# Optimization experiments

Hardware: AMD Instinct MI355X
Metric: run time of the kernel (lower is better)

## Reference

```python
import jax, jax.numpy as jnp
import numpy as np

T, B, K, H = 2048, 4, 512, 8  # seq_len, batch, num_features, num_heads


def setup_inputs() -> dict:
    key = jax.random.key(0)
    ks = jax.random.split(key, 9)
    s_in = 1.0 / np.sqrt(K).astype(np.float32)       # torch Linear init bound (fan_in = K)
    s_out = 1.0 / np.sqrt(H * K).astype(np.float32)  # fan_in = H*K for output linear
    u = lambda k, shape, s: jax.random.uniform(k, shape, jnp.float32, -s, s)
    return {
        "x": jax.random.normal(ks[0], (T, B, K), jnp.float32),
        "Wq": u(ks[1], (K, H * K), s_in), "bq": u(ks[2], (H * K,), s_in),
        "Wk": u(ks[3], (K, H * K), s_in), "bk": u(ks[4], (H * K,), s_in),
        "Wv": u(ks[5], (K, H * K), s_in), "bv": u(ks[6], (H * K,), s_in),
        "Wo": u(ks[7], (H * K, H), s_out), "bo": u(ks[8], (H,), s_out),
    }


def reference(x, Wq, bq, Wk, bk, Wv, bv, Wo, bo):
    t, b, k = x.shape
    h = Wq.shape[1] // k
    scale = k ** -0.25  # q and k each scaled by num_features**(1/4) -> net 1/sqrt(k)
    # QKV projections: (t, b, h*k) -> view as (t, b*h, k) like the torch .view
    q = ((jnp.einsum('tbk,kf->tbf', x, Wq) + bq) * scale).reshape(t, b * h, k)
    ky = ((jnp.einsum('tbk,kf->tbf', x, Wk) + bk) * scale).reshape(t, b * h, k)
    v = (jnp.einsum('tbk,kf->tbf', x, Wv) + bv).reshape(t, b * h, k)
    # per-(batch*head) slice attention, vectorized over the b*h axis n
    scores = jnp.einsum('tnk,snk->nts', q, ky)          # (b*h, t, t)
    attn = jax.nn.softmax(scores, axis=-1)
    ctx = jnp.einsum('nts,snk->tnk', attn, v).reshape(t, b, h * k)
    return jnp.einsum('tbf,fo->tbo', ctx, Wo) + bo      # (t, b, h)
```

## Files before the change

### kernel.cpp

```cpp
#include <hip/hip_runtime.h>
#include <hip/hip_bf16.h>
#include <stdint.h>


typedef __bf16 bf16_t;
typedef __bf16 bf16x8 __attribute__((ext_vector_type(8)));
using short8 = __attribute__((ext_vector_type(8))) short;
typedef float  f32x4  __attribute__((ext_vector_type(4)));
typedef uint32_t u32;

#define T_N 2048
#define K_N 512
#define F_N 4096
#define SCALE_QK 0.21022410381342863f

#define AS3 __attribute__((address_space(3)))
#define AS1 __attribute__((address_space(1)))

__device__ __forceinline__ void gll16(const void* gsrc, void* ldst) {
  __builtin_amdgcn_global_load_lds((const AS1 u32*)gsrc, (AS3 u32*)ldst, 16, 0, 0);
}

__global__ void prep_x(const float* __restrict__ x, bf16_t* __restrict__ xb) {
  int i = (blockIdx.x * 256 + threadIdx.x) * 8;
  float4 a = *(const float4*)(x + i);
  float4 b = *(const float4*)(x + i + 4);
  bf16x8 o;
  o[0] = (bf16_t)a.x; o[1] = (bf16_t)a.y; o[2] = (bf16_t)a.z; o[3] = (bf16_t)a.w;
  o[4] = (bf16_t)b.x; o[5] = (bf16_t)b.y; o[6] = (bf16_t)b.z; o[7] = (bf16_t)b.w;
  *(bf16x8*)(xb + i) = o;
}

__global__ void prep_w(const float* __restrict__ Wq, const float* __restrict__ Wk,
                       const float* __restrict__ Wv, bf16_t* __restrict__ Wt) {
  const float* W = blockIdx.z == 0 ? Wq : (blockIdx.z == 1 ? Wk : Wv);
  bf16_t* out = Wt + (size_t)blockIdx.z * F_N * K_N;
  __shared__ alignas(16) bf16_t tile[64][72];
  int k0 = blockIdx.x * 64, f0 = blockIdx.y * 64;
  int tid = threadIdx.x;
  int r = tid >> 3, cc = (tid & 7) * 8;
#pragma unroll
  for (int h = 0; h < 2; h++) {
    int rr = r + h * 32;
    const float* src = W + (size_t)(k0 + rr) * F_N + f0 + cc;
    float4 a = *(const float4*)src;
    float4 b = *(const float4*)(src + 4);
    bf16_t* d = &tile[rr][cc];
    d[0] = (bf16_t)a.x; d[1] = (bf16_t)a.y; d[2] = (bf16_t)a.z; d[3] = (bf16_t)a.w;
    d[4] = (bf16_t)b.x; d[5] = (bf16_t)b.y; d[6] = (bf16_t)b.z; d[7] = (bf16_t)b.w;
  }
  __syncthreads();
#pragma unroll
  for (int h = 0; h < 2; h++) {
    int rr = r + h * 32;
    bf16x8 o;
#pragma unroll
    for (int j = 0; j < 8; j++) o[j] = tile[cc + j][rr];
    *(bf16x8*)(out + (size_t)(f0 + rr) * K_N + k0 + cc) = o;
  }
}

__global__ void zero_l(float* l) { l[blockIdx.x * 256 + threadIdx.x] = 0.0f; }

template <int CHH>
__global__ void transpose_v_t(const bf16_t* __restrict__ Vc, bf16_t* __restrict__ Vtc) {
  constexpr int CW = CHH * 512;
  int zc = blockIdx.z, b = zc & 3, hh = zc >> 2;
  int t0 = blockIdx.x * 64, d0 = blockIdx.y * 64;
  __shared__ alignas(16) bf16_t tile[64][72];
  int tid = threadIdx.x;
  int r = tid >> 3, cc = (tid & 7) * 8;
#pragma unroll
  for (int h = 0; h < 2; h++) {
    int rr = r + h * 32;
    *(bf16x8*)&tile[rr][cc] = *(const bf16x8*)(
        Vc + (size_t)(t0 + rr) * 4 * CW + (size_t)b * CW + hh * 512 + d0 + cc);
  }
  __syncthreads();
  bf16_t* out = Vtc + (size_t)zc * K_N * T_N;
#pragma unroll
  for (int h = 0; h < 2; h++) {
    int rr = r + h * 32;
    bf16x8 o;
#pragma unroll
    for (int j = 0; j < 8; j++) o[j] = tile[cc + j][rr];
    *(bf16x8*)(out + (size_t)(d0 + rr) * T_N + t0 + cc) = o;
  }
}

struct GemmAcc { f32x4 a[4][4]; };

__device__ __forceinline__ void gemm_bt_core(
    const char* __restrict__ Ab, size_t sA, const char* __restrict__ Bb, size_t sB,
    int mbase, int nbase, int NK, char* smem, GemmAcc& G) {
  const int tid = threadIdx.x;
  const int lane = tid & 63;
  const int wid = tid >> 6;
#pragma unroll
  for (int i = 0; i < 4; i++)
#pragma unroll
    for (int j = 0; j < 4; j++) G.a[i][j] = f32x4{0.f, 0.f, 0.f, 0.f};

  const int rsub = lane >> 3;
  const int qb = (lane & 7) * 16;

  auto stage = [&](int buf, int kt) {
    char* base = smem + buf * 32768;
#pragma unroll
    for (int it = 0; it < 4; it++) {
      int r = wid * 32 + it * 8 + rsub;
      const char* src = Ab + (size_t)(mbase + r) * sA + kt * 128 + (qb ^ ((r & 7) << 4));
      gll16(src, base + wid * 4096 + it * 1024);
    }
#pragma unroll
    for (int it = 0; it < 4; it++) {
      int r = wid * 32 + it * 8 + rsub;
      const char* src = Bb + (size_t)(nbase + r) * sB + kt * 128 + (qb ^ ((r & 7) << 4));
      gll16(src, base + 16384 + wid * 4096 + it * 1024);
    }
  };

  const int wm = wid >> 1, wn = wid & 1;
  const int rl = lane & 15;
  const int kg = (lane >> 4) * 16;

  auto compute = [&](int buf) {
    const char* base = smem + buf * 32768;
#pragma unroll
    for (int kf = 0; kf < 2; kf++) {
      int kb = kf * 64 + kg;
      short8 af[4], bfv[4];
#pragma unroll
      for (int mf = 0; mf < 4; mf++) {
        int m = wm * 64 + mf * 16 + rl;
        af[mf] = *(const short8*)(base + m * 128 + (kb ^ ((m & 7) << 4)));
      }
#pragma unroll
      for (int nf = 0; nf < 4; nf++) {
        int n = wn * 64 + nf * 16 + rl;
        bfv[nf] = *(const short8*)(base + 16384 + n * 128 + (kb ^ ((n & 7) << 4)));
      }
#pragma unroll
      for (int mf = 0; mf < 4; mf++)
#pragma unroll
        for (int nf = 0; nf < 4; nf++)
          G.a[mf][nf] = __builtin_amdgcn_mfma_f32_16x16x32_bf16(af[mf], bfv[nf],
                                                                G.a[mf][nf], 0, 0, 0);
    }
  };

  stage(0, 0);
  for (int kt = 0; kt < NK; kt++) {
    __syncthreads();
    if (kt + 1 < NK) stage((kt + 1) & 1, kt + 1);
    compute(kt & 1);
  }
}

#define EPILOGUE_COORDS                                   \
  const int lane = threadIdx.x & 63;                      \
  const int wid = threadIdx.x >> 6;                       \
  const int wm = wid >> 1, wn = wid & 1;                  \
  const int cl = lane & 15;                               \
  const int rg = (lane >> 4) * 4;

template <int CHH>
__global__ __launch_bounds__(256, 2) void gemm_proj_t(
    const bf16_t* __restrict__ xb, const bf16_t* __restrict__ Wt,
    bf16_t* __restrict__ Qc, bf16_t* __restrict__ Kc, bf16_t* __restrict__ Vc,
    const float* __restrict__ bq, const float* __restrict__ bk,
    const float* __restrict__ bv, int h0) {
  constexpr int CW = CHH * 512;
  __shared__ alignas(16) char smem[65536];
  int z = blockIdx.z;
  const char* Ab = (const char*)xb;
  const char* Bb = (const char*)(Wt + ((size_t)z * F_N + h0 * 512) * K_N);
  int mbase = blockIdx.x * 128, nbase = blockIdx.y * 128;
  GemmAcc G;
  gemm_bt_core(Ab, 1024, Bb, 1024, mbase, nbase, 8, smem, G);

  bf16_t* C = z == 0 ? Qc : (z == 1 ? Kc : Vc);
  const float* bias = z == 0 ? bq : (z == 1 ? bk : bv);
  float scale = z < 2 ? SCALE_QK : 1.0f;
  EPILOGUE_COORDS
#pragma unroll
  for (int nf = 0; nf < 4; nf++) {
    int col = nbase + wn * 64 + nf * 16 + cl;
    float bvv = bias[h0 * 512 + col];
#pragma unroll
    for (int mf = 0; mf < 4; mf++)
#pragma unroll
      for (int ri = 0; ri < 4; ri++) {
        int row = mbase + wm * 64 + mf * 16 + rg + ri;
        C[(size_t)row * CW + col] = (bf16_t)((G.a[mf][nf][ri] + bvv) * scale);
      }
  }
}

template <int CHH>
__global__ __launch_bounds__(256, 2) void gemm_s_t(
    const bf16_t* __restrict__ Qc, const bf16_t* __restrict__ Kc,
    bf16_t* __restrict__ E, float* __restrict__ L, int h0, int zb) {
  constexpr int CW = CHH * 512;
  __shared__ alignas(16) char smem[65536];
  int ze = blockIdx.z;
  int zc = zb + ze, b = zc & 3, hh = zc >> 2;
  const char* Ab = (const char*)(Qc + (size_t)(b * CHH + hh) * 512);
  const char* Bb = (const char*)(Kc + (size_t)(b * CHH + hh) * 512);
  int mbase = blockIdx.x * 128, nbase = blockIdx.y * 128;
  GemmAcc G;
  gemm_bt_core(Ab, 8 * CW, Bb, 8 * CW, mbase, nbase, 8, smem, G);

  bf16_t* C = E + (size_t)ze * T_N * T_N;
  float* Ln = L + ((h0 + hh) * 4 + b) * T_N;
  EPILOGUE_COORDS
#pragma unroll
  for (int mf = 0; mf < 4; mf++)
#pragma unroll
    for (int ri = 0; ri < 4; ri++) {
      int row = mbase + wm * 64 + mf * 16 + rg + ri;
      float rs = 0.0f;
#pragma unroll
      for (int nf = 0; nf < 4; nf++) {
        int col = nbase + wn * 64 + nf * 16 + cl;
        float e = __expf(G.a[mf][nf][ri]);
        rs += e;
        C[(size_t)row * T_N + col] = (bf16_t)e;
      }
#pragma unroll
      for (int off = 1; off < 16; off <<= 1) rs += __shfl_xor(rs, off, 16);
      if ((lane & 15) == 0) atomicAdd(Ln + row, rs);
    }
}

template <int CHH>
__global__ __launch_bounds__(256, 2) void gemm_pv_t(
    const bf16_t* __restrict__ E, const bf16_t* __restrict__ Vtc,
    const float* __restrict__ L, bf16_t* __restrict__ ctxc, int h0, int zb) {
  constexpr int CW = CHH * 512;
  __shared__ alignas(16) char smem[65536];
  int ze = blockIdx.z;
  int zc = zb + ze, b = zc & 3, hh = zc >> 2;
  const char* Ab = (const char*)(E + (size_t)ze * T_N * T_N);
  const char* Bb = (const char*)(Vtc + (size_t)zc * K_N * T_N);
  int mbase = blockIdx.x * 128, nbase = blockIdx.y * 128;
  GemmAcc G;
  gemm_bt_core(Ab, 4096, Bb, 4096, mbase, nbase, 32, smem, G);

  const float* Ln = L + ((h0 + hh) * 4 + b) * T_N;
  bf16_t* C = ctxc + (size_t)(b * CHH + hh) * 512;
  EPILOGUE_COORDS
#pragma unroll
  for (int mf = 0; mf < 4; mf++)
#pragma unroll
    for (int ri = 0; ri < 4; ri++) {
      int row = mbase + wm * 64 + mf * 16 + rg + ri;
      float inv = 1.0f / Ln[row];
#pragma unroll
      for (int nf = 0; nf < 4; nf++) {
        int col = nbase + wn * 64 + nf * 16 + cl;
        C[(size_t)row * 4 * CW + col] = (bf16_t)(G.a[mf][nf][ri] * inv);
      }
    }
}

template <int CHH>
__global__ __launch_bounds__(256) void out_gemm_t(
    const bf16_t* __restrict__ ctxc, const float* __restrict__ Wo,
    const float* __restrict__ bo, float* __restrict__ out, int h0, int first) {
  constexpr int CW = CHH * 512;
  int tid = threadIdx.x, lane = tid & 63, wid = tid >> 6;
  int r = blockIdx.x * 4 + wid;
  const bf16_t* crow = ctxc + (size_t)r * CW + lane * (8 * CHH);
  const float* wbase = Wo + ((size_t)h0 * 512 + lane * (8 * CHH)) * 8;
  float p[8];
#pragma unroll
  for (int o = 0; o < 8; o++) p[o] = 0.0f;
#pragma unroll
  for (int j = 0; j < 8 * CHH; j += 8) {
    bf16x8 cv = *(const bf16x8*)(crow + j);
#pragma unroll
    for (int u = 0; u < 8; u++) {
      float c = (float)cv[u];
      const float* wrow = wbase + (j + u) * 8;
      f32x4 w0 = *(const f32x4*)wrow;
      f32x4 w1 = *(const f32x4*)(wrow + 4);
      p[0] += c * w0[0]; p[1] += c * w0[1]; p[2] += c * w0[2]; p[3] += c * w0[3];
      p[4] += c * w1[0]; p[5] += c * w1[1]; p[6] += c * w1[2]; p[7] += c * w1[3];
    }
  }
#pragma unroll
  for (int off = 1; off < 64; off <<= 1)
#pragma unroll
    for (int o = 0; o < 8; o++) p[o] += __shfl_xor(p[o], off, 64);
  if (lane == 0) {
#pragma unroll
    for (int o = 0; o < 8; o++) {
      float base = first ? bo[o] : out[r * 8 + o];
      out[r * 8 + o] = base + p[o];
    }
  }
}

template <int CHH>
static void run_chunks(const bf16_t* xb, const bf16_t* Wt, bf16_t* Qc, bf16_t* Kc,
                       bf16_t* Vc, bf16_t* Vtc, bf16_t* ctxc, bf16_t* E, float* L,
                       const float* bq, const float* bk, const float* bv,
                       const float* Wo, const float* bo, float* out, int NZ,
                       hipStream_t stream) {
  constexpr int CW = CHH * 512;
  for (int c = 0; c < 8 / CHH; c++) {
    int h0 = c * CHH;
    gemm_proj_t<CHH><<<dim3(64, CW / 128, 3), 256, 0, stream>>>(
        xb, Wt, Qc, Kc, Vc, bq, bk, bv, h0);
    transpose_v_t<CHH><<<dim3(32, 8, 4 * CHH), 256, 0, stream>>>(Vc, Vtc);
    for (int zb = 0; zb < 4 * CHH; zb += NZ) {
      gemm_s_t<CHH><<<dim3(16, 16, NZ), 256, 0, stream>>>(Qc, Kc, E, L, h0, zb);
      gemm_pv_t<CHH><<<dim3(16, 4, NZ), 256, 0, stream>>>(E, Vtc, L, ctxc, h0, zb);
    }
    out_gemm_t<CHH><<<2048, 256, 0, stream>>>(ctxc, Wo, bo, out, h0, c == 0);
  }
}

extern "C" void kernel_launch(void* const* d_in, const int* in_sizes, int n_in,
                              void* d_out, int out_size, void* d_ws, size_t ws_size,
                              hipStream_t stream) {
  const float* x  = (const float*)d_in[0];
  const float* Wq = (const float*)d_in[1];
  const float* bq = (const float*)d_in[2];
  const float* Wk = (const float*)d_in[3];
  const float* bk = (const float*)d_in[4];
  const float* Wv = (const float*)d_in[5];
  const float* bv = (const float*)d_in[6];
  const float* Wo = (const float*)d_in[7];
  const float* bo = (const float*)d_in[8];
  float* out = (float*)d_out;
  char* ws = (char*)d_ws;

  const size_t MiB = 1ull << 20;
  int CHH, NZ;
  if      (ws_size >= 309 * MiB) { CHH = 4; NZ = 16; }
  else if (ws_size >= 165 * MiB) { CHH = 2; NZ = 8;  }
  else if (ws_size >= 93  * MiB) { CHH = 1; NZ = 4;  }
  else                           { CHH = 1; NZ = 1;  }

  size_t SZ = (size_t)CHH * 8 * MiB;
  bf16_t* xb   = (bf16_t*)(ws);
  bf16_t* Wt   = (bf16_t*)(ws + 8 * MiB);
  bf16_t* Qc   = (bf16_t*)(ws + 20 * MiB);
  bf16_t* Kc   = (bf16_t*)(ws + 20 * MiB + SZ);
  bf16_t* Vc   = (bf16_t*)(ws + 20 * MiB + 2 * SZ);
  bf16_t* Vtc  = (bf16_t*)(ws + 20 * MiB + 3 * SZ);
  bf16_t* ctxc = (bf16_t*)(ws + 20 * MiB + 4 * SZ);
  bf16_t* E    = (bf16_t*)(ws + 20 * MiB + 5 * SZ);
  float*  L    = (float*) (ws + 20 * MiB + 5 * SZ + (size_t)NZ * 8 * MiB);

  prep_x<<<2048, 256, 0, stream>>>(x, xb);
  prep_w<<<dim3(8, 64, 3), 256, 0, stream>>>(Wq, Wk, Wv, Wt);
  zero_l<<<256, 256, 0, stream>>>(L);

  if (CHH == 4)
    run_chunks<4>(xb, Wt, Qc, Kc, Vc, Vtc, ctxc, E, L, bq, bk, bv, Wo, bo, out, NZ, stream);
  else if (CHH == 2)
    run_chunks<2>(xb, Wt, Qc, Kc, Vc, Vtc, ctxc, E, L, bq, bk, bv, Wo, bo, out, NZ, stream);
  else
    run_chunks<1>(xb, Wt, Qc, Kc, Vc, Vtc, ctxc, E, L, bq, bk, bv, Wo, bo, out, NZ, stream);
}
```

Measured before the change: 706.8 us.

## Use 256x256 eight-wave pipelined GEMM core for projection and score kernels

Adds a new GEMM core that uses 256x256 tiles with 8 waves, a double-buffered 128KB LDS, XOR-swizzled layout, explicit vmcnt/lgkmcnt waits, barriers and s_setprio around MFMA phases. This interleaves global-to-LDS loads with compute. The projection and QK^T/exp kernels now use it in place of the 128x128 four-wave core. The aim is more data reuse per tile and better overlap of loads with MFMA work. In exchange the grids are smaller, LDS use is larger (lower occupancy), and the hand-scheduled sync is more fragile.

```diff
diff --git a/kernel.cpp b/kernel.cpp
--- a/kernel.cpp
+++ b/kernel.cpp
@@ -20,6 +20,14 @@
 __device__ __forceinline__ void gll16(const void* gsrc, void* ldst) {
   __builtin_amdgcn_global_load_lds((const AS1 u32*)gsrc, (AS3 u32*)ldst, 16, 0, 0);
 }
+
+#define SB   __builtin_amdgcn_s_barrier()
+#define WLG  do { asm volatile("s_waitcnt lgkmcnt(0)" ::: "memory"); \
+                  __builtin_amdgcn_sched_barrier(0); } while (0)
+#define PRI1 __builtin_amdgcn_s_setprio(1)
+#define PRI0 __builtin_amdgcn_s_setprio(0)
+#define VM6  asm volatile("s_waitcnt vmcnt(6)" ::: "memory")
+#define VM0  asm volatile("s_waitcnt vmcnt(0)" ::: "memory")
 
 __global__ void prep_x(const float* __restrict__ x, bf16_t* __restrict__ xb) {
   int i = (blockIdx.x * 256 + threadIdx.x) * 8;
@@ -88,6 +96,187 @@
   }
 }
 
+template <int NKT>
+__device__ __forceinline__ void gemm_bt_8ph(
+    const char* __restrict__ Ab, int sA, const char* __restrict__ Bb, int sB,
+    int mbase, int nbase, char* smem, f32x4 (&acc)[8][4]) {
+  static_assert(NKT >= 4 && (NKT & 1) == 0, "NKT even >= 4");
+  const int lane = threadIdx.x & 63;
+  const int wid  = threadIdx.x >> 6;
+  const int wr   = wid >> 2, wc = wid & 3;
+  const int rl   = lane & 15;
+  const int kg   = (lane >> 4) * 16;
+  const int sx   = (rl & 7) << 4;
+  const int srow = lane >> 3;
+  const int scol = (lane & 7) * 16;
+  const int sxs  = srow << 4;
+
+#pragma unroll
+  for (int i = 0; i < 8; i++)
+#pragma unroll
+    for (int j = 0; j < 4; j++) acc[i][j] = f32x4{0.f, 0.f, 0.f, 0.f};
+
+  auto STG = [&](int mat, int half, int kt) {
+    if (kt >= NKT) return;
+    char* dst = smem + (kt & 1) * 65536 + mat * 32768 + half * 16384 + wid * 1024;
+    const char* gb = mat ? Bb : Ab;
+    int s = mat ? sB : sA;
+    int rb = (mat ? nbase : mbase) + half * 128;
+#pragma unroll
+    for (int j = 0; j < 2; j++) {
+      int r = j * 64 + wid * 8 + srow;
+      gll16(gb + (size_t)(rb + r) * s + kt * 128 + (scol ^ sxs), dst + j * 8192);
+    }
+  };
+
+  short8 aF[4][2], bF0[2][2], bF1[2][2];
+  auto LDA = [&](int mh, const char* bufA) {
+#pragma unroll
+    for (int j = 0; j < 4; j++) {
+      int m = mh * 128 + wr * 64 + j * 16 + rl;
+#pragma unroll
+      for (int ks = 0; ks < 2; ks++)
+        aF[j][ks] = *(const short8*)(bufA + m * 128 + ((ks * 64 + kg) ^ sx));
+    }
+  };
+  auto LDB = [&](short8 (&bF)[2][2], int nh, const char* bufB) {
+#pragma unroll
+    for (int j2 = 0; j2 < 2; j2++) {
+      int n = nh * 128 + wc * 32 + j2 * 16 + rl;
+#pragma unroll
+      for (int ks = 0; ks < 2; ks++)
+        bF[j2][ks] = *(const short8*)(bufB + n * 128 + ((ks * 64 + kg) ^ sx));
+    }
+  };
+  auto MM = [&](int mh, int nh, short8 (&bF)[2][2]) {
+#pragma unroll
+    for (int j = 0; j < 4; j++)
+#pragma unroll
+      for (int j2 = 0; j2 < 2; j2++)
+#pragma unroll
+        for (int ks = 0; ks < 2; ks++)
+          acc[mh * 4 + j][nh * 2 + j2] = __builtin_amdgcn_mfma_f32_16x16x32_bf16(
+              aF[j][ks], bF[j2][ks], acc[mh * 4 + j][nh * 2 + j2], 0, 0, 0);
+  };
+
+  const char* A0 = smem;
+  const char* B0 = smem + 32768;
+  const char* A1 = smem + 65536;
+  const char* B1 = smem + 65536 + 32768;
+
+  STG(0, 0, 0); STG(1, 0, 0); STG(1, 1, 0); STG(0, 1, 0);
+  STG(0, 0, 1); STG(1, 0, 1); STG(1, 1, 1);
+  VM6; SB;
+
+#pragma unroll 1
+  for (int t0 = 0; t0 < NKT; t0 += 2) {
+    const bool more = (t0 + 2 < NKT);
+    LDA(0, A0); LDB(bF0, 0, B0); STG(0, 1, t0 + 1);
+    SB; WLG; PRI1; MM(0, 0, bF0); PRI0; SB;
+    LDB(bF1, 1, B0); STG(0, 0, t0 + 2);
+    SB; WLG; PRI1; MM(0, 1, bF1); PRI0; SB;
+    LDA(1, A0); STG(1, 0, t0 + 2);
+    SB; WLG; PRI1; MM(1, 1, bF1); PRI0; SB;
+    STG(1, 1, t0 + 2);
+    if (more) { VM6; } else { VM0; }
+    SB; WLG; PRI1; MM(1, 0, bF0); PRI0; SB;
+    LDA(0, A1); LDB(bF0, 0, B1); STG(0, 1, t0 + 2);
+    SB; WLG; PRI1; MM(0, 0, bF0); PRI0; SB;
+    LDB(bF1, 1, B1); STG(0, 0, t0 + 3);
+    SB; WLG; PRI1; MM(0, 1, bF1); PRI0; SB;
+    LDA(1, A1); STG(1, 0, t0 + 3);
+    SB; WLG; PRI1; MM(1, 1, bF1); PRI0; SB;
+    STG(1, 1, t0 + 3);
+    if (t0 + 3 < NKT) { VM6; } else { VM0; }
+    SB; WLG; PRI1; MM(1, 0, bF0); PRI0; SB;
+  }
+}
+
+#define EPI8_COORDS                                       \
+  const int lane = threadIdx.x & 63;                      \
+  const int wid = threadIdx.x >> 6;                       \
+  const int wr = wid >> 2, wc = wid & 3;                  \
+  const int cl = lane & 15;                               \
+  const int rg = (lane >> 4) * 4;
+
+template <int CHH>
+__global__ __launch_bounds__(512, 2) void gemm_proj8_t(
+    const bf16_t* __restrict__ xb, const bf16_t* __restrict__ Wt,
+    bf16_t* __restrict__ Qc, bf16_t* __restrict__ Kc, bf16_t* __restrict__ Vc,
+    const float* __restrict__ bq, const float* __restrict__ bk,
+    const float* __restrict__ bv, int h0) {
+  constexpr int CW = CHH * 512;
+  extern __shared__ __align__(16) char dsm[];
+  int z = blockIdx.z;
+  const char* Ab = (const char*)xb;
+  const char* Bb = (const char*)(Wt + ((size_t)z * F_N + h0 * 512) * K_N);
+  int mbase = blockIdx.x * 256, nbase = blockIdx.y * 256;
+  f32x4 acc[8][4];
+  gemm_bt_8ph<8>(Ab, 1024, Bb, 1024, mbase, nbase, dsm, acc);
+
+  bf16_t* C = z == 0 ? Qc : (z == 1 ? Kc : Vc);
+  const float* bias = z == 0 ? bq : (z == 1 ? bk : bv);
+  float scale = z < 2 ? SCALE_QK : 1.0f;
+  EPI8_COORDS
+#pragma unroll
+  for (int nh = 0; nh < 2; nh++)
+#pragma unroll
+    for (int j2 = 0; j2 < 2; j2++) {
+      int col = nbase + nh * 128 + wc * 32 + j2 * 16 + cl;
+      float bvv = bias[h0 * 512 + col];
+#pragma unroll
+      for (int mh = 0; mh < 2; mh++)
+#pragma unroll
+        for (int j = 0; j < 4; j++)
+#pragma unroll
+          for (int ri = 0; ri < 4; ri++) {
+            int row = mbase + mh * 128 + wr * 64 + j * 16 + rg + ri;
+            C[(size_t)row * CW + col] =
+                (bf16_t)((acc[mh * 4 + j][nh * 2 + j2][ri] + bvv) * scale);
+          }
+    }
+}
+
+template <int CHH>
+__global__ __launch_bounds__(512, 2) void gemm_s8_t(
+    const bf16_t* __restrict__ Qc, const bf16_t* __restrict__ Kc,
+    bf16_t* __restrict__ E, float* __restrict__ L, int h0, int zb) {
+  constexpr int CW = CHH * 512;
+  extern __shared__ __align__(16) char dsm[];
+  int ze = blockIdx.z;
+  int zc = zb + ze, b = zc & 3, hh = zc >> 2;
+  const char* Ab = (const char*)(Qc + (size_t)(b * CHH + hh) * 512);
+  const char* Bb = (const char*)(Kc + (size_t)(b * CHH + hh) * 512);
+  int mbase = blockIdx.x * 256, nbase = blockIdx.y * 256;
+  f32x4 acc[8][4];
+  gemm_bt_8ph<8>(Ab, 8 * CW, Bb, 8 * CW, mbase, nbase, dsm, acc);
+
+  bf16_t* C = E + (size_t)ze * T_N * T_N;
+  float* Ln = L + ((h0 + hh) * 4 + b) * T_N;
+  EPI8_COORDS
+#pragma unroll
+  for (int mh = 0; mh < 2; mh++)
+#pragma unroll
+    for (int j = 0; j < 4; j++)
+#pragma unroll
+      for (int ri = 0; ri < 4; ri++) {
+        int row = mbase + mh * 128 + wr * 64 + j * 16 + rg + ri;
+        float rs = 0.0f;
+#pragma unroll
+        for (int nh = 0; nh < 2; nh++)
+#pragma unroll
+          for (int j2 = 0; j2 < 2; j2++) {
+            int col = nbase + nh * 128 + wc * 32 + j2 * 16 + cl;
+            float e = __expf(acc[mh * 4 + j][nh * 2 + j2][ri]);
+            rs += e;
+            C[(size_t)row * T_N + col] = (bf16_t)e;
+          }
+#pragma unroll
+        for (int off = 1; off < 16; off <<= 1) rs += __shfl_xor(rs, off, 16);
+        if ((lane & 15) == 0) atomicAdd(Ln + row, rs);
+      }
+}
+
 struct GemmAcc { f32x4 a[4][4]; };
 
 __device__ __forceinline__ void gemm_bt_core(
@@ -163,75 +352,6 @@
   const int wm = wid >> 1, wn = wid & 1;                  \
   const int cl = lane & 15;                               \
   const int rg = (lane >> 4) * 4;
-
-template <int CHH>
-__global__ __launch_bounds__(256, 2) void gemm_proj_t(
-    const bf16_t* __restrict__ xb, const bf16_t* __restrict__ Wt,
-    bf16_t* __restrict__ Qc, bf16_t* __restrict__ Kc, bf16_t* __restrict__ Vc,
-    const float* __restrict__ bq, const float* __restrict__ bk,
-    const float* __restrict__ bv, int h0) {
-  constexpr int CW = CHH * 512;
-  __shared__ alignas(16) char smem[65536];
-  int z = blockIdx.z;
-  const char* Ab = (const char*)xb;
-  const char* Bb = (const char*)(Wt + ((size_t)z * F_N + h0 * 512) * K_N);
-  int mbase = blockIdx.x * 128, nbase = blockIdx.y * 128;
-  GemmAcc G;
-  gemm_bt_core(Ab, 1024, Bb, 1024, mbase, nbase, 8, smem, G);
-
-  bf16_t* C = z == 0 ? Qc : (z == 1 ? Kc : Vc);
-  const float* bias = z == 0 ? bq : (z == 1 ? bk : bv);
-  float scale = z < 2 ? SCALE_QK : 1.0f;
-  EPILOGUE_COORDS
-#pragma unroll
-  for (int nf = 0; nf < 4; nf++) {
-    int col = nbase + wn * 64 + nf * 16 + cl;
-    float bvv = bias[h0 * 512 + col];
-#pragma unroll
-    for (int mf = 0; mf < 4; mf++)
-#pragma unroll
-      for (int ri = 0; ri < 4; ri++) {
-        int row = mbase + wm * 64 + mf * 16 + rg + ri;
-        C[(size_t)row * CW + col] = (bf16_t)((G.a[mf][nf][ri] + bvv) * scale);
-      }
-  }
-}
-
-template <int CHH>
-__global__ __launch_bounds__(256, 2) void gemm_s_t(
-    const bf16_t* __restrict__ Qc, const bf16_t* __restrict__ Kc,
-    bf16_t* __restrict__ E, float* __restrict__ L, int h0, int zb) {
-  constexpr int CW = CHH * 512;
-  __shared__ alignas(16) char smem[65536];
-  int ze = blockIdx.z;
-  int zc = zb + ze, b = zc & 3, hh = zc >> 2;
-  const char* Ab = (const char*)(Qc + (size_t)(b * CHH + hh) * 512);
-  const char* Bb = (const char*)(Kc + (size_t)(b * CHH + hh) * 512);
-  int mbase = blockIdx.x * 128, nbase = blockIdx.y * 128;
-  GemmAcc G;
-  gemm_bt_core(Ab, 8 * CW, Bb, 8 * CW, mbase, nbase, 8, smem, G);
-
-  bf16_t* C = E + (size_t)ze * T_N * T_N;
-  float* Ln = L + ((h0 + hh) * 4 + b) * T_N;
-  EPILOGUE_COORDS
-#pragma unroll
-  for (int mf = 0; mf < 4; mf++)
-#pragma unroll
-    for (int ri = 0; ri < 4; ri++) {
-      int row = mbase + wm * 64 + mf * 16 + rg + ri;
-      float rs = 0.0f;
-#pragma unroll
-      for (int nf = 0; nf < 4; nf++) {
-        int col = nbase + wn * 64 + nf * 16 + cl;
-        float e = __expf(G.a[mf][nf][ri]);
-        rs += e;
-        C[(size_t)row * T_N + col] = (bf16_t)e;
-      }
-#pragma unroll
-      for (int off = 1; off < 16; off <<= 1) rs += __shfl_xor(rs, off, 16);
-      if ((lane & 15) == 0) atomicAdd(Ln + row, rs);
-    }
-}
 
 template <int CHH>
 __global__ __launch_bounds__(256, 2) void gemm_pv_t(
@@ -309,13 +429,17 @@
                        const float* Wo, const float* bo, float* out, int NZ,
                        hipStream_t stream) {
   constexpr int CW = CHH * 512;
+  hipFuncSetAttribute(reinterpret_cast<const void*>(gemm_proj8_t<CHH>),
+                      hipFuncAttributeMaxDynamicSharedMemorySize, 131072);
+  hipFuncSetAttribute(reinterpret_cast<const void*>(gemm_s8_t<CHH>),
+                      hipFuncAttributeMaxDynamicSharedMemorySize, 131072);
   for (int c = 0; c < 8 / CHH; c++) {
     int h0 = c * CHH;
-    gemm_proj_t<CHH><<<dim3(64, CW / 128, 3), 256, 0, stream>>>(
+    gemm_proj8_t<CHH><<<dim3(32, CW / 256, 3), 512, 131072, stream>>>(
         xb, Wt, Qc, Kc, Vc, bq, bk, bv, h0);
     transpose_v_t<CHH><<<dim3(32, 8, 4 * CHH), 256, 0, stream>>>(Vc, Vtc);
     for (int zb = 0; zb < 4 * CHH; zb += NZ) {
-      gemm_s_t<CHH><<<dim3(16, 16, NZ), 256, 0, stream>>>(Qc, Kc, E, L, h0, zb);
+      gemm_s8_t<CHH><<<dim3(8, 8, NZ), 512, 131072, stream>>>(Qc, Kc, E, L, h0, zb);
       gemm_pv_t<CHH><<<dim3(16, 4, NZ), 256, 0, stream>>>(E, Vtc, L, ctxc, h0, zb);
     }
     out_gemm_t<CHH><<<2048, 256, 0, stream>>>(ctxc, Wo, bo, out, h0, c == 0);
```

After: 794.9 us. 12.5% more time.

## Chain multiple short-K GEMMs per block with continuous double-buffered pipeline

Applied to the files above, without the earlier changes.

Adds a chained GEMM core that runs J independent K=512 GEMMs back-to-back in one block, keeping the double-buffered global-to-LDS prefetch running across GEMM boundaries and emitting each tile's epilogue in between. The QKV projection now does Q, K and V in one block (grid z from 3 to 1), and the score GEMM processes 4 heads per block when NZ allows. This is meant to amortize pipeline fill/drain and launch overhead of the short K loops, at the cost of fewer blocks (less parallelism) and serialized epilogues.

```diff
diff --git a/kernel.cpp b/kernel.cpp
--- a/kernel.cpp
+++ b/kernel.cpp
@@ -90,16 +90,91 @@
 
 struct GemmAcc { f32x4 a[4][4]; };
 
+#define GEMM_ZERO(G)                                        \
+  _Pragma("unroll") for (int i_ = 0; i_ < 4; i_++)          \
+  _Pragma("unroll") for (int j_ = 0; j_ < 4; j_++)          \
+      G.a[i_][j_] = f32x4{0.f, 0.f, 0.f, 0.f};
+
+template <int SA, int SB, int J, typename PanFn, typename EpiFn>
+__device__ __forceinline__ void gemm_bt_chain8(
+    PanFn pan, EpiFn epi, int mbase, int nbase, char* smem) {
+  const int tid = threadIdx.x;
+  const int lane = tid & 63;
+  const int wid = tid >> 6;
+  GemmAcc G;
+  GEMM_ZERO(G)
+
+  const int rsub = lane >> 3;
+  const int qb = (lane & 7) * 16;
+
+  auto stage = [&](int s) {
+    int j = s >> 3, kt = s & 7;
+    char* base = smem + (s & 1) * 32768;
+    const char* Ab = pan(j, 0);
+    const char* Bb = pan(j, 1);
+#pragma unroll
+    for (int it = 0; it < 4; it++) {
+      int r = wid * 32 + it * 8 + rsub;
+      gll16(Ab + (size_t)(mbase + r) * SA + kt * 128 + (qb ^ ((r & 7) << 4)),
+            base + wid * 4096 + it * 1024);
+    }
+#pragma unroll
+    for (int it = 0; it < 4; it++) {
+      int r = wid * 32 + it * 8 + rsub;
+      gll16(Bb + (size_t)(nbase + r) * SB + kt * 128 + (qb ^ ((r & 7) << 4)),
+            base + 16384 + wid * 4096 + it * 1024);
+    }
+  };
+
+  const int wm = wid >> 1, wn = wid & 1;
+  const int rl = lane & 15;
+  const int kg = (lane >> 4) * 16;
+
+  auto compute = [&](int buf) {
+    const char* base = smem + buf * 32768;
+#pragma unroll
+    for (int kf = 0; kf < 2; kf++) {
+      int kb = kf * 64 + kg;
+      short8 af[4], bfv[4];
+#pragma unroll
+      for (int mf = 0; mf < 4; mf++) {
+        int m = wm * 64 + mf * 16 + rl;
+        af[mf] = *(const short8*)(base + m * 128 + (kb ^ ((m & 7) << 4)));
+      }
+#pragma unroll
+      for (int nf = 0; nf < 4; nf++) {
+        int n = wn * 64 + nf * 16 + rl;
+        bfv[nf] = *(const short8*)(base + 16384 + n * 128 + (kb ^ ((n & 7) << 4)));
+      }
+#pragma unroll
+      for (int mf = 0; mf < 4; mf++)
+#pragma unroll
+        for (int nf = 0; nf < 4; nf++)
+          G.a[mf][nf] = __builtin_amdgcn_mfma_f32_16x16x32_bf16(af[mf], bfv[nf],
+                                                                G.a[mf][nf], 0, 0, 0);
+    }
+  };
+
+  stage(0);
+#pragma unroll 1
+  for (int s = 0; s < J * 8; s++) {
+    __syncthreads();
+    if (s + 1 < J * 8) stage(s + 1);
+    compute(s & 1);
+    if ((s & 7) == 7) {
+      epi(s >> 3, G);
+      GEMM_ZERO(G)
+    }
+  }
+}
+
 __device__ __forceinline__ void gemm_bt_core(
     const char* __restrict__ Ab, size_t sA, const char* __restrict__ Bb, size_t sB,
     int mbase, int nbase, int NK, char* smem, GemmAcc& G) {
   const int tid = threadIdx.x;
   const int lane = tid & 63;
   const int wid = tid >> 6;
-#pragma unroll
-  for (int i = 0; i < 4; i++)
-#pragma unroll
-    for (int j = 0; j < 4; j++) G.a[i][j] = f32x4{0.f, 0.f, 0.f, 0.f};
+  GEMM_ZERO(G)
 
   const int rsub = lane >> 3;
   const int qb = (lane & 7) * 16;
@@ -172,65 +247,73 @@
     const float* __restrict__ bv, int h0) {
   constexpr int CW = CHH * 512;
   __shared__ alignas(16) char smem[65536];
-  int z = blockIdx.z;
-  const char* Ab = (const char*)xb;
-  const char* Bb = (const char*)(Wt + ((size_t)z * F_N + h0 * 512) * K_N);
   int mbase = blockIdx.x * 128, nbase = blockIdx.y * 128;
-  GemmAcc G;
-  gemm_bt_core(Ab, 1024, Bb, 1024, mbase, nbase, 8, smem, G);
-
-  bf16_t* C = z == 0 ? Qc : (z == 1 ? Kc : Vc);
-  const float* bias = z == 0 ? bq : (z == 1 ? bk : bv);
-  float scale = z < 2 ? SCALE_QK : 1.0f;
   EPILOGUE_COORDS
-#pragma unroll
-  for (int nf = 0; nf < 4; nf++) {
-    int col = nbase + wn * 64 + nf * 16 + cl;
-    float bvv = bias[h0 * 512 + col];
-#pragma unroll
-    for (int mf = 0; mf < 4; mf++)
-#pragma unroll
-      for (int ri = 0; ri < 4; ri++) {
-        int row = mbase + wm * 64 + mf * 16 + rg + ri;
-        C[(size_t)row * CW + col] = (bf16_t)((G.a[mf][nf][ri] + bvv) * scale);
-      }
-  }
-}
-
-template <int CHH>
+
+  auto pan = [&](int j, int isB) -> const char* {
+    if (!isB) return (const char*)xb;
+    return (const char*)(Wt + ((size_t)j * F_N + h0 * 512) * K_N);
+  };
+  auto epi = [&](int j, GemmAcc& G) {
+    bf16_t* C = j == 0 ? Qc : (j == 1 ? Kc : Vc);
+    const float* bias = j == 0 ? bq : (j == 1 ? bk : bv);
+    float scale = j < 2 ? SCALE_QK : 1.0f;
+#pragma unroll
+    for (int nf = 0; nf < 4; nf++) {
+      int col = nbase + wn * 64 + nf * 16 + cl;
+      float bvv = bias[h0 * 512 + col];
+#pragma unroll
+      for (int mf = 0; mf < 4; mf++)
+#pragma unroll
+        for (int ri = 0; ri < 4; ri++) {
+          int row = mbase + wm * 64 + mf * 16 + rg + ri;
+          C[(size_t)row * CW + col] = (bf16_t)((G.a[mf][nf][ri] + bvv) * scale);
+        }
+    }
+  };
+  gemm_bt_chain8<1024, 1024, 3>(pan, epi, mbase, nbase, smem);
+}
+
+template <int CHH, int J>
 __global__ __launch_bounds__(256, 2) void gemm_s_t(
     const bf16_t* __restrict__ Qc, const bf16_t* __restrict__ Kc,
     bf16_t* __restrict__ E, float* __restrict__ L, int h0, int zb) {
   constexpr int CW = CHH * 512;
   __shared__ alignas(16) char smem[65536];
-  int ze = blockIdx.z;
-  int zc = zb + ze, b = zc & 3, hh = zc >> 2;
-  const char* Ab = (const char*)(Qc + (size_t)(b * CHH + hh) * 512);
-  const char* Bb = (const char*)(Kc + (size_t)(b * CHH + hh) * 512);
+  int ze0 = blockIdx.z * J;
   int mbase = blockIdx.x * 128, nbase = blockIdx.y * 128;
-  GemmAcc G;
-  gemm_bt_core(Ab, 8 * CW, Bb, 8 * CW, mbase, nbase, 8, smem, G);
-
-  bf16_t* C = E + (size_t)ze * T_N * T_N;
-  float* Ln = L + ((h0 + hh) * 4 + b) * T_N;
   EPILOGUE_COORDS
-#pragma unroll
-  for (int mf = 0; mf < 4; mf++)
-#pragma unroll
-    for (int ri = 0; ri < 4; ri++) {
-      int row = mbase + wm * 64 + mf * 16 + rg + ri;
-      float rs = 0.0f;
-#pragma unroll
-      for (int nf = 0; nf < 4; nf++) {
-        int col = nbase + wn * 64 + nf * 16 + cl;
-        float e = __expf(G.a[mf][nf][ri]);
-        rs += e;
-        C[(size_t)row * T_N + col] = (bf16_t)e;
-      }
-#pragma unroll
-      for (int off = 1; off < 16; off <<= 1) rs += __shfl_xor(rs, off, 16);
-      if ((lane & 15) == 0) atomicAdd(Ln + row, rs);
-    }
+
+  auto pan = [&](int j, int isB) -> const char* {
+    int zc = zb + ze0 + j;
+    int b = zc & 3, hh = zc >> 2;
+    const bf16_t* base = isB ? Kc : Qc;
+    return (const char*)(base + (size_t)(b * CHH + hh) * 512);
+  };
+  auto epi = [&](int j, GemmAcc& G) {
+    int ze = ze0 + j;
+    int zc = zb + ze, b = zc & 3, hh = zc >> 2;
+    bf16_t* C = E + (size_t)ze * T_N * T_N;
+    float* Ln = L + ((h0 + hh) * 4 + b) * T_N;
+#pragma unroll
+    for (int mf = 0; mf < 4; mf++)
+#pragma unroll
+      for (int ri = 0; ri < 4; ri++) {
+        int row = mbase + wm * 64 + mf * 16 + rg + ri;
+        float rs = 0.0f;
+#pragma unroll
+        for (int nf = 0; nf < 4; nf++) {
+          int col = nbase + wn * 64 + nf * 16 + cl;
+          float e = __expf(G.a[mf][nf][ri]);
+          rs += e;
+          C[(size_t)row * T_N + col] = (bf16_t)e;
+        }
+#pragma unroll
+        for (int off = 1; off < 16; off <<= 1) rs += __shfl_xor(rs, off, 16);
+        if ((lane & 15) == 0) atomicAdd(Ln + row, rs);
+      }
+  };
+  gemm_bt_chain8<8 * CW, 8 * CW, J>(pan, epi, mbase, nbase, smem);
 }
 
 template <int CHH>
@@ -311,11 +394,14 @@
   constexpr int CW = CHH * 512;
   for (int c = 0; c < 8 / CHH; c++) {
     int h0 = c * CHH;
-    gemm_proj_t<CHH><<<dim3(64, CW / 128, 3), 256, 0, stream>>>(
+    gemm_proj_t<CHH><<<dim3(64, CW / 128, 1), 256, 0, stream>>>(
         xb, Wt, Qc, Kc, Vc, bq, bk, bv, h0);
     transpose_v_t<CHH><<<dim3(32, 8, 4 * CHH), 256, 0, stream>>>(Vc, Vtc);
     for (int zb = 0; zb < 4 * CHH; zb += NZ) {
-      gemm_s_t<CHH><<<dim3(16, 16, NZ), 256, 0, stream>>>(Qc, Kc, E, L, h0, zb);
+      if (NZ >= 4)
+        gemm_s_t<CHH, 4><<<dim3(16, 16, NZ / 4), 256, 0, stream>>>(Qc, Kc, E, L, h0, zb);
+      else
+        gemm_s_t<CHH, 1><<<dim3(16, 16, NZ), 256, 0, stream>>>(Qc, Kc, E, L, h0, zb);
       gemm_pv_t<CHH><<<dim3(16, 4, NZ), 256, 0, stream>>>(E, Vtc, L, ctxc, h0, zb);
     }
     out_gemm_t<CHH><<<2048, 256, 0, stream>>>(ctxc, Wo, bo, out, h0, c == 0);
```

New measurement: 803.4 us. 13.7% more time.
